# Kernel optimization log

Measured on AMD Instinct MI355X. Metric: run time of the kernel, lower is better.

## Reference

```python
import jax, jax.numpy as jnp
import numpy as np

N_NODES = 100000
N_EDGES = 1200000
IN_FEATS = 64
OUT_FEATS = 32
K_HOPS = 4  # k = len([in_feats] + hidden_lst) with hidden_lst=[64,64,32]


def setup_inputs() -> dict:
    key = jax.random.key(0)
    k1, k2, k3, k4, k5 = jax.random.split(key, 5)
    features = jax.random.normal(k1, (N_NODES, IN_FEATS), dtype=jnp.float32)
    src = jax.random.randint(k2, (N_EDGES,), 0, N_NODES, dtype=jnp.int64)
    dst = jax.random.randint(k3, (N_EDGES,), 0, N_NODES, dtype=jnp.int64)
    # fc layer of SGConv: Linear(in_feats -> out_feats) with bias
    bound = 1.0 / np.sqrt(IN_FEATS)
    W = jax.random.uniform(k4, (OUT_FEATS, IN_FEATS), dtype=jnp.float32,
                           minval=-bound, maxval=bound)
    b = jax.random.uniform(k5, (OUT_FEATS,), dtype=jnp.float32,
                           minval=-bound, maxval=bound)
    return {"features": features, "src": src, "dst": dst, "W": W, "b": b}


def reference(features, src, dst, W, b):
    # DGL SGConv with norm='both': symmetric normalization each hop.
    # in-degree of each dst node, clamped to >= 1
    deg = jax.ops.segment_sum(jnp.ones((N_EDGES,), dtype=features.dtype),
                              dst, num_segments=N_NODES)
    norm = jnp.clip(deg, 1.0, None) ** -0.5  # [N]
    norm = norm[:, None]                      # [N, 1]
    h = features
    for _ in range(K_HOPS):
        h = h * norm                                            # D^{-1/2} x
        h = jax.ops.segment_sum(h[src], dst, num_segments=N_NODES)  # A x (SpMM)
        h = h * norm                                            # D^{-1/2}
    # final linear layer
    return h @ W.T + b
```

## Files before the change

### kernel.cpp

```cpp
#include <hip/hip_runtime.h>
#include <hip/hip_fp16.h>
#include <cstdint>

#define NNODES 100000
#define NEDGES 1200000
#define INF 64
#define OUTF 32
#define SCAN_B 256
#define NBUCK ((NNODES + SCAN_B - 1) / SCAN_B)
#define PCAP 4608
#define PADCAP 5632
#define BIN_EPT 16
#define BIN_THREADS (NEDGES / BIN_EPT)
#define BIN_BLOCKS ((BIN_THREADS + 255) / 256)
#define PROJ_NPB 16
#define PROJ_BLOCKS (NNODES / PROJ_NPB)
#define CUR_PAD 16
#define WST 66

__global__ __launch_bounds__(256) void k_initcur(int* __restrict__ gcur,
                                                 uint4* __restrict__ h0,
                                                 uint4* __restrict__ h1) {
    int i = blockIdx.x * 256 + threadIdx.x;
    if (i < NBUCK) gcur[i * CUR_PAD] = i * PCAP;
    if (i >= 256 && i < 260) h0[(size_t)NNODES * 4 + (i - 256)] = make_uint4(0, 0, 0, 0);
    if (i >= 260 && i < 264) h1[(size_t)NNODES * 4 + (i - 260)] = make_uint4(0, 0, 0, 0);
}

__global__ __launch_bounds__(256) void k_binproj(const int4* __restrict__ src4,
                                                 const int4* __restrict__ dst4,
                                                 int* __restrict__ gcur,
                                                 unsigned* __restrict__ packed,
                                                 const float4* __restrict__ feat4,
                                                 const float4* __restrict__ W4,
                                                 __half2* __restrict__ h0_p) {
    __shared__ __align__(16) char smem[12672];
    int tid = threadIdx.x;
    if (blockIdx.x < BIN_BLOCKS) {
        int* cnt = (int*)smem;
        int* base = cnt + NBUCK;
        for (int i = tid; i < NBUCK; i += 256) cnt[i] = 0;
        __syncthreads();
        int gid = blockIdx.x * 256 + tid;
        bool act = gid < BIN_THREADS;
        int4 s4[4], d4[4];
        if (act) {
#pragma unroll
            for (int k = 0; k < 4; ++k) {
                s4[k] = src4[(size_t)gid * 4 + k];
                d4[k] = dst4[(size_t)gid * 4 + k];
                atomicAdd(&cnt[d4[k].x >> 8], 1);
                atomicAdd(&cnt[d4[k].y >> 8], 1);
                atomicAdd(&cnt[d4[k].z >> 8], 1);
                atomicAdd(&cnt[d4[k].w >> 8], 1);
            }
        }
        __syncthreads();
        for (int i = tid; i < NBUCK; i += 256) {
            int c = cnt[i];
            base[i] = c ? atomicAdd(&gcur[i * CUR_PAD], c) : 0;
            cnt[i] = 0;
        }
        __syncthreads();
        if (act) {
#pragma unroll
            for (int k = 0; k < 4; ++k) {
                int ss[4] = {s4[k].x, s4[k].y, s4[k].z, s4[k].w};
                int dd[4] = {d4[k].x, d4[k].y, d4[k].z, d4[k].w};
#pragma unroll
                for (int j = 0; j < 4; ++j) {
                    int b = dd[j] >> 8;
                    int rel = atomicAdd(&cnt[b], 1);
                    packed[base[b] + rel] =
                        ((unsigned)(dd[j] & 255) << 17) | (unsigned)ss[j];
                }
            }
        }
    } else {
        float (*Ws)[WST] = (float (*)[WST])smem;
        float (*Fs)[WST] = (float (*)[WST])(smem + 32 * WST * 4);
        int node0 = (blockIdx.x - BIN_BLOCKS) * PROJ_NPB;
        for (int i = tid; i < 512; i += 256) {
            float4 w = W4[i];
            int f = i * 4, of = f >> 6, k = f & 63;
            Ws[of][k] = w.x; Ws[of][k + 1] = w.y;
            Ws[of][k + 2] = w.z; Ws[of][k + 3] = w.w;
        }
        {
            int n = node0 + (tid >> 4), q = tid & 15;
            float4 v = feat4[(size_t)n * 16 + q];
            int c = q * 4;
            Fs[tid >> 4][c] = v.x; Fs[tid >> 4][c + 1] = v.y;
            Fs[tid >> 4][c + 2] = v.z; Fs[tid >> 4][c + 3] = v.w;
        }
        __syncthreads();
        int ln = tid >> 4, n = node0 + ln;
        int of0 = (tid & 15) * 2;
        const float2* fp = (const float2*)&Fs[ln][0];
        const float2* w0 = (const float2*)&Ws[of0][0];
        const float2* w1 = (const float2*)&Ws[of0 + 1][0];
        float a0 = 0.0f, a1 = 0.0f;
#pragma unroll
        for (int k2 = 0; k2 < 32; ++k2) {
            float2 f = fp[k2], x = w0[k2], y = w1[k2];
            a0 += f.x * x.x + f.y * x.y;
            a1 += f.x * y.x + f.y * y.y;
        }
        h0_p[(size_t)n * 16 + (tid & 15)] = __floats2half2_rn(a0, a1);
    }
}

__global__ __launch_bounds__(256) void k_place(const unsigned* __restrict__ packed,
                                               const int* __restrict__ gcur,
                                               int* __restrict__ col,
                                               unsigned* __restrict__ rowsd,
                                               float* __restrict__ norm,
                                               uint4* __restrict__ h0) {
    __shared__ unsigned sin_[PCAP];
    __shared__ int stage[PADCAP];
    __shared__ int deg[SCAN_B];
    __shared__ int rs[SCAN_B];
    __shared__ int cur[SCAN_B];
    __shared__ int tot;
    int b = blockIdx.x, tid = threadIdx.x;
    int node0 = b * SCAN_B;
    int nn = (NNODES - node0 < SCAN_B) ? (NNODES - node0) : SCAN_B;
    int ebase = b * PCAP;
    int pbase = b * PADCAP;
    int nedge = gcur[b * CUR_PAD] - ebase;
    deg[tid] = 0;
    __syncthreads();
    for (int i = tid; i < nedge; i += 256) {
        unsigned pk = packed[ebase + i];
        sin_[i] = pk;
        atomicAdd(&deg[pk >> 17], 1);
    }
    __syncthreads();
    int d = deg[tid];
    int dpad = (d + 7) & ~7;
    rs[tid] = dpad;
    __syncthreads();
    for (int st = 1; st < SCAN_B; st <<= 1) {
        int add = (tid >= st) ? rs[tid - st] : 0;
        __syncthreads();
        rs[tid] += add;
        __syncthreads();
    }
    int myoff = rs[tid] - dpad;
    if (tid == SCAN_B - 1) tot = rs[tid];
    float mynorm = rsqrtf(d < 1 ? 1.0f : (float)d);
    if (tid < nn) {
        norm[node0 + tid] = mynorm;
        rowsd[node0 + tid] =
            ((unsigned)((pbase + myoff) >> 3) << 9) | (unsigned)(dpad >> 3);
    }
    cur[tid] = myoff;
    __syncthreads();
    for (int i = tid; i < tot; i += 256) stage[i] = NNODES;
    __syncthreads();
    for (int i = tid; i < nedge; i += 256) {
        unsigned pk = sin_[i];
        int rel = atomicAdd(&cur[pk >> 17], 1);
        stage[rel] = (int)(pk & 0x1FFFFu);
    }
    __syncthreads();
    for (int i = tid; i < tot; i += 256) col[pbase + i] = stage[i];
    if (tid < nn) {
        uint4* hp = h0 + (size_t)(node0 + tid) * 4;
#pragma unroll
        for (int k = 0; k < 4; ++k) {
            uint4 r = hp[k];
            float2 f0 = __half22float2(*(const __half2*)&r.x);
            float2 f1 = __half22float2(*(const __half2*)&r.y);
            float2 f2 = __half22float2(*(const __half2*)&r.z);
            float2 f3 = __half22float2(*(const __half2*)&r.w);
            *(__half2*)&r.x = __floats2half2_rn(mynorm * f0.x, mynorm * f0.y);
            *(__half2*)&r.y = __floats2half2_rn(mynorm * f1.x, mynorm * f1.y);
            *(__half2*)&r.z = __floats2half2_rn(mynorm * f2.x, mynorm * f2.y);
            *(__half2*)&r.w = __floats2half2_rn(mynorm * f3.x, mynorm * f3.y);
            hp[k] = r;
        }
    }
}

template <bool LAST>
__global__ __launch_bounds__(256) void k_gather(const uint4* __restrict__ uin,
                                                void* __restrict__ uout,
                                                const unsigned* __restrict__ rowsd,
                                                const int4* __restrict__ colv,
                                                const float* __restrict__ norm,
                                                const float4* __restrict__ bias4) {
    int t = blockIdx.x * 256 + threadIdx.x;
    int node = t >> 2;
    if (node >= NNODES) return;
    int lane = t & 3;
    unsigned rd = rowsd[node];
    int c4 = (int)(rd >> 9) * 2;
    int n8 = (int)(rd & 511u);
    const uint4* up = uin + lane;
    float4 accA = make_float4(0.f, 0.f, 0.f, 0.f);
    float4 accB = make_float4(0.f, 0.f, 0.f, 0.f);
    auto add = [&](uint4 r) {
        float2 f0 = __half22float2(*(const __half2*)&r.x);
        float2 f1 = __half22float2(*(const __half2*)&r.y);
        float2 f2 = __half22float2(*(const __half2*)&r.z);
        float2 f3 = __half22float2(*(const __half2*)&r.w);
        accA.x += f0.x; accA.y += f0.y; accA.z += f1.x; accA.w += f1.y;
        accB.x += f2.x; accB.y += f2.y; accB.z += f3.x; accB.w += f3.y;
    };
    for (int j = 0; j < n8; ++j) {
        int4 c0 = colv[c4 + j * 2];
        int4 c1 = colv[c4 + j * 2 + 1];
        uint4 r0 = up[(size_t)c0.x * 4];
        uint4 r1 = up[(size_t)c0.y * 4];
        uint4 r2 = up[(size_t)c0.z * 4];
        uint4 r3 = up[(size_t)c0.w * 4];
        uint4 r4 = up[(size_t)c1.x * 4];
        uint4 r5 = up[(size_t)c1.y * 4];
        uint4 r6 = up[(size_t)c1.z * 4];
        uint4 r7 = up[(size_t)c1.w * 4];
        add(r0); add(r1); add(r2); add(r3);
        add(r4); add(r5); add(r6); add(r7);
    }
    float nn = norm[node];
    float w = LAST ? nn : nn * nn;
    accA.x *= w; accA.y *= w; accA.z *= w; accA.w *= w;
    accB.x *= w; accB.y *= w; accB.z *= w; accB.w *= w;
    if (LAST) {
        float4 b0 = bias4[lane * 2], b1 = bias4[lane * 2 + 1];
        accA.x += b0.x; accA.y += b0.y; accA.z += b0.z; accA.w += b0.w;
        accB.x += b1.x; accB.y += b1.y; accB.z += b1.z; accB.w += b1.w;
        float4* o = (float4*)uout;
        o[(size_t)node * 8 + lane * 2]     = accA;
        o[(size_t)node * 8 + lane * 2 + 1] = accB;
    } else {
        uint4 r;
        *(__half2*)&r.x = __floats2half2_rn(accA.x, accA.y);
        *(__half2*)&r.y = __floats2half2_rn(accA.z, accA.w);
        *(__half2*)&r.z = __floats2half2_rn(accB.x, accB.y);
        *(__half2*)&r.w = __floats2half2_rn(accB.z, accB.w);
        ((uint4*)uout)[(size_t)node * 4 + lane] = r;
    }
}

extern "C" void kernel_launch(void* const* d_in, const int* in_sizes, int n_in,
                              void* d_out, int out_size, void* d_ws, size_t ws_size,
                              hipStream_t stream) {
    const float* feat = (const float*)d_in[0];
    const int*   src  = (const int*)d_in[1];
    const int*   dst  = (const int*)d_in[2];
    const float* W    = (const float*)d_in[3];
    const float* b    = (const float*)d_in[4];
    float* out = (float*)d_out;

    char* ws = (char*)d_ws;
    size_t off = 0;
    auto alloc = [&](size_t bytes) {
        void* p = ws + off;
        off = (off + bytes + 255) & ~(size_t)255;
        return p;
    };
    float*    norm   = (float*)alloc((size_t)NNODES * 4);
    unsigned* rowsd  = (unsigned*)alloc((size_t)NNODES * 4);
    int*      gcur   = (int*)alloc((size_t)NBUCK * CUR_PAD * 4);
    unsigned* packed = (unsigned*)alloc((size_t)NBUCK * PCAP * 4);
    int*      col    = (int*)alloc((size_t)NBUCK * PADCAP * 4);
    void*     h0     = alloc((size_t)(NNODES + 1) * OUTF * 2);
    void*     h1     = alloc((size_t)(NNODES + 1) * OUTF * 2);

    k_initcur<<<2, 256, 0, stream>>>(gcur, (uint4*)h0, (uint4*)h1);
    k_binproj<<<BIN_BLOCKS + PROJ_BLOCKS, 256, 0, stream>>>(
        (const int4*)src, (const int4*)dst, gcur, packed,
        (const float4*)feat, (const float4*)W, (__half2*)h0);
    k_place<<<NBUCK, 256, 0, stream>>>(packed, gcur, col, rowsd, norm,
                                       (uint4*)h0);

    const int ggrid = (NNODES * 4 + 255) / 256;
    k_gather<false><<<ggrid, 256, 0, stream>>>(
        (const uint4*)h0, h1, rowsd, (const int4*)col, norm, nullptr);
    k_gather<false><<<ggrid, 256, 0, stream>>>(
        (const uint4*)h1, h0, rowsd, (const int4*)col, norm, nullptr);
    k_gather<false><<<ggrid, 256, 0, stream>>>(
        (const uint4*)h0, h1, rowsd, (const int4*)col, norm, nullptr);
    k_gather<true><<<ggrid, 256, 0, stream>>>(
        (const uint4*)h1, out, rowsd, (const int4*)col, norm, (const float4*)b);
}
```

Before: 119.6 us.

## Restage binning through shared memory and fuse projection with CSR placement

Binning now stages packed edges in shared memory, grouped per bucket, and writes them to global memory in contiguous runs instead of scattered stores. The feature projection moves from the binning kernel into the placement kernel, so it runs alongside CSR construction. The first gather applies the source norm per edge through a norm lookup, with a zero sentinel for padding, so the placement kernel no longer rescales h0. This aims to cut scattered writes and one read-modify-write pass over h0, at the cost of extra norm loads in the first hop and more shared memory in the binning kernel.

```diff
diff --git a/kernel.cpp b/kernel.cpp
--- a/kernel.cpp
+++ b/kernel.cpp
@@ -20,66 +20,131 @@
 
 __global__ __launch_bounds__(256) void k_initcur(int* __restrict__ gcur,
                                                  uint4* __restrict__ h0,
-                                                 uint4* __restrict__ h1) {
+                                                 uint4* __restrict__ h1,
+                                                 float* __restrict__ norm) {
     int i = blockIdx.x * 256 + threadIdx.x;
     if (i < NBUCK) gcur[i * CUR_PAD] = i * PCAP;
     if (i >= 256 && i < 260) h0[(size_t)NNODES * 4 + (i - 256)] = make_uint4(0, 0, 0, 0);
     if (i >= 260 && i < 264) h1[(size_t)NNODES * 4 + (i - 260)] = make_uint4(0, 0, 0, 0);
-}
-
-__global__ __launch_bounds__(256) void k_binproj(const int4* __restrict__ src4,
-                                                 const int4* __restrict__ dst4,
-                                                 int* __restrict__ gcur,
-                                                 unsigned* __restrict__ packed,
-                                                 const float4* __restrict__ feat4,
-                                                 const float4* __restrict__ W4,
-                                                 __half2* __restrict__ h0_p) {
-    __shared__ __align__(16) char smem[12672];
+    if (i == 264) norm[NNODES] = 0.0f;
+}
+
+__global__ __launch_bounds__(256) void k_bin(const int4* __restrict__ src4,
+                                             const int4* __restrict__ dst4,
+                                             int* __restrict__ gcur,
+                                             unsigned* __restrict__ packed) {
+    __shared__ int cnt[NBUCK];
+    __shared__ int base[NBUCK];
+    __shared__ int loff[NBUCK];
+    __shared__ int ltot;
+    __shared__ unsigned sval[4096];
+    __shared__ int saddr[4096];
     int tid = threadIdx.x;
-    if (blockIdx.x < BIN_BLOCKS) {
-        int* cnt = (int*)smem;
-        int* base = cnt + NBUCK;
-        for (int i = tid; i < NBUCK; i += 256) cnt[i] = 0;
-        __syncthreads();
-        int gid = blockIdx.x * 256 + tid;
-        bool act = gid < BIN_THREADS;
-        int4 s4[4], d4[4];
-        if (act) {
-#pragma unroll
-            for (int k = 0; k < 4; ++k) {
-                s4[k] = src4[(size_t)gid * 4 + k];
-                d4[k] = dst4[(size_t)gid * 4 + k];
-                atomicAdd(&cnt[d4[k].x >> 8], 1);
-                atomicAdd(&cnt[d4[k].y >> 8], 1);
-                atomicAdd(&cnt[d4[k].z >> 8], 1);
-                atomicAdd(&cnt[d4[k].w >> 8], 1);
+    for (int i = tid; i < NBUCK; i += 256) cnt[i] = 0;
+    if (tid == 0) ltot = 0;
+    __syncthreads();
+    int gid = blockIdx.x * 256 + tid;
+    bool act = gid < BIN_THREADS;
+    int4 s4[4], d4[4];
+    if (act) {
+#pragma unroll
+        for (int k = 0; k < 4; ++k) {
+            s4[k] = src4[(size_t)gid * 4 + k];
+            d4[k] = dst4[(size_t)gid * 4 + k];
+            atomicAdd(&cnt[d4[k].x >> 8], 1);
+            atomicAdd(&cnt[d4[k].y >> 8], 1);
+            atomicAdd(&cnt[d4[k].z >> 8], 1);
+            atomicAdd(&cnt[d4[k].w >> 8], 1);
+        }
+    }
+    __syncthreads();
+    for (int i = tid; i < NBUCK; i += 256) {
+        int c = cnt[i];
+        if (c) {
+            base[i] = atomicAdd(&gcur[i * CUR_PAD], c);
+            loff[i] = atomicAdd(&ltot, c);
+        }
+        cnt[i] = 0;
+    }
+    __syncthreads();
+    if (act) {
+#pragma unroll
+        for (int k = 0; k < 4; ++k) {
+            int ss[4] = {s4[k].x, s4[k].y, s4[k].z, s4[k].w};
+            int dd[4] = {d4[k].x, d4[k].y, d4[k].z, d4[k].w};
+#pragma unroll
+            for (int j = 0; j < 4; ++j) {
+                int b = dd[j] >> 8;
+                int rel = atomicAdd(&cnt[b], 1);
+                int p = loff[b] + rel;
+                sval[p] = ((unsigned)(dd[j] & 255) << 17) | (unsigned)ss[j];
+                saddr[p] = base[b] + rel;
             }
         }
-        __syncthreads();
-        for (int i = tid; i < NBUCK; i += 256) {
-            int c = cnt[i];
-            base[i] = c ? atomicAdd(&gcur[i * CUR_PAD], c) : 0;
-            cnt[i] = 0;
-        }
-        __syncthreads();
-        if (act) {
-#pragma unroll
-            for (int k = 0; k < 4; ++k) {
-                int ss[4] = {s4[k].x, s4[k].y, s4[k].z, s4[k].w};
-                int dd[4] = {d4[k].x, d4[k].y, d4[k].z, d4[k].w};
-#pragma unroll
-                for (int j = 0; j < 4; ++j) {
-                    int b = dd[j] >> 8;
-                    int rel = atomicAdd(&cnt[b], 1);
-                    packed[base[b] + rel] =
-                        ((unsigned)(dd[j] & 255) << 17) | (unsigned)ss[j];
-                }
-            }
-        }
+    }
+    __syncthreads();
+    int tot = ltot;
+    for (int i = tid; i < tot; i += 256) packed[saddr[i]] = sval[i];
+}
+
+__global__ __launch_bounds__(256) void k_placeproj(const unsigned* __restrict__ packed,
+                                                   const int* __restrict__ gcur,
+                                                   int* __restrict__ col,
+                                                   unsigned* __restrict__ rowsd,
+                                                   float* __restrict__ norm,
+                                                   const float4* __restrict__ feat4,
+                                                   const float4* __restrict__ W4,
+                                                   __half2* __restrict__ h0_p) {
+    __shared__ __align__(16) char smem[25664];
+    int tid = threadIdx.x;
+    if (blockIdx.x < NBUCK) {
+        int* stage = (int*)smem;
+        int* deg   = (int*)(smem + 22528);
+        int* rs    = (int*)(smem + 23552);
+        int* cur   = (int*)(smem + 24576);
+        int b = blockIdx.x;
+        int node0 = b * SCAN_B;
+        int nn = (NNODES - node0 < SCAN_B) ? (NNODES - node0) : SCAN_B;
+        int ebase = b * PCAP;
+        int pbase = b * PADCAP;
+        int nedge = gcur[b * CUR_PAD] - ebase;
+        deg[tid] = 0;
+        __syncthreads();
+        for (int i = tid; i < nedge; i += 256)
+            atomicAdd(&deg[packed[ebase + i] >> 17], 1);
+        __syncthreads();
+        int d = deg[tid];
+        int dpad = (d + 7) & ~7;
+        rs[tid] = dpad;
+        __syncthreads();
+        for (int st = 1; st < SCAN_B; st <<= 1) {
+            int add = (tid >= st) ? rs[tid - st] : 0;
+            __syncthreads();
+            rs[tid] += add;
+            __syncthreads();
+        }
+        int myoff = rs[tid] - dpad;
+        if (tid < nn) {
+            norm[node0 + tid] = rsqrtf(d < 1 ? 1.0f : (float)d);
+            rowsd[node0 + tid] =
+                ((unsigned)((pbase + myoff) >> 3) << 9) | (unsigned)(dpad >> 3);
+        }
+        cur[tid] = myoff;
+        __syncthreads();
+        int totp = rs[SCAN_B - 1];
+        for (int i = tid; i < totp; i += 256) stage[i] = NNODES;
+        __syncthreads();
+        for (int i = tid; i < nedge; i += 256) {
+            unsigned pk = packed[ebase + i];
+            int rel = atomicAdd(&cur[pk >> 17], 1);
+            stage[rel] = (int)(pk & 0x1FFFFu);
+        }
+        __syncthreads();
+        for (int i = tid; i < totp; i += 256) col[pbase + i] = stage[i];
     } else {
         float (*Ws)[WST] = (float (*)[WST])smem;
         float (*Fs)[WST] = (float (*)[WST])(smem + 32 * WST * 4);
-        int node0 = (blockIdx.x - BIN_BLOCKS) * PROJ_NPB;
+        int node0 = (blockIdx.x - NBUCK) * PROJ_NPB;
         for (int i = tid; i < 512; i += 256) {
             float4 w = W4[i];
             int f = i * 4, of = f >> 6, k = f & 63;
@@ -110,80 +175,7 @@
     }
 }
 
-__global__ __launch_bounds__(256) void k_place(const unsigned* __restrict__ packed,
-                                               const int* __restrict__ gcur,
-                                               int* __restrict__ col,
-                                               unsigned* __restrict__ rowsd,
-                                               float* __restrict__ norm,
-                                               uint4* __restrict__ h0) {
-    __shared__ unsigned sin_[PCAP];
-    __shared__ int stage[PADCAP];
-    __shared__ int deg[SCAN_B];
-    __shared__ int rs[SCAN_B];
-    __shared__ int cur[SCAN_B];
-    __shared__ int tot;
-    int b = blockIdx.x, tid = threadIdx.x;
-    int node0 = b * SCAN_B;
-    int nn = (NNODES - node0 < SCAN_B) ? (NNODES - node0) : SCAN_B;
-    int ebase = b * PCAP;
-    int pbase = b * PADCAP;
-    int nedge = gcur[b * CUR_PAD] - ebase;
-    deg[tid] = 0;
-    __syncthreads();
-    for (int i = tid; i < nedge; i += 256) {
-        unsigned pk = packed[ebase + i];
-        sin_[i] = pk;
-        atomicAdd(&deg[pk >> 17], 1);
-    }
-    __syncthreads();
-    int d = deg[tid];
-    int dpad = (d + 7) & ~7;
-    rs[tid] = dpad;
-    __syncthreads();
-    for (int st = 1; st < SCAN_B; st <<= 1) {
-        int add = (tid >= st) ? rs[tid - st] : 0;
-        __syncthreads();
-        rs[tid] += add;
-        __syncthreads();
-    }
-    int myoff = rs[tid] - dpad;
-    if (tid == SCAN_B - 1) tot = rs[tid];
-    float mynorm = rsqrtf(d < 1 ? 1.0f : (float)d);
-    if (tid < nn) {
-        norm[node0 + tid] = mynorm;
-        rowsd[node0 + tid] =
-            ((unsigned)((pbase + myoff) >> 3) << 9) | (unsigned)(dpad >> 3);
-    }
-    cur[tid] = myoff;
-    __syncthreads();
-    for (int i = tid; i < tot; i += 256) stage[i] = NNODES;
-    __syncthreads();
-    for (int i = tid; i < nedge; i += 256) {
-        unsigned pk = sin_[i];
-        int rel = atomicAdd(&cur[pk >> 17], 1);
-        stage[rel] = (int)(pk & 0x1FFFFu);
-    }
-    __syncthreads();
-    for (int i = tid; i < tot; i += 256) col[pbase + i] = stage[i];
-    if (tid < nn) {
-        uint4* hp = h0 + (size_t)(node0 + tid) * 4;
-#pragma unroll
-        for (int k = 0; k < 4; ++k) {
-            uint4 r = hp[k];
-            float2 f0 = __half22float2(*(const __half2*)&r.x);
-            float2 f1 = __half22float2(*(const __half2*)&r.y);
-            float2 f2 = __half22float2(*(const __half2*)&r.z);
-            float2 f3 = __half22float2(*(const __half2*)&r.w);
-            *(__half2*)&r.x = __floats2half2_rn(mynorm * f0.x, mynorm * f0.y);
-            *(__half2*)&r.y = __floats2half2_rn(mynorm * f1.x, mynorm * f1.y);
-            *(__half2*)&r.z = __floats2half2_rn(mynorm * f2.x, mynorm * f2.y);
-            *(__half2*)&r.w = __floats2half2_rn(mynorm * f3.x, mynorm * f3.y);
-            hp[k] = r;
-        }
-    }
-}
-
-template <bool LAST>
+template <bool FIRST, bool LAST>
 __global__ __launch_bounds__(256) void k_gather(const uint4* __restrict__ uin,
                                                 void* __restrict__ uout,
                                                 const unsigned* __restrict__ rowsd,
@@ -200,13 +192,13 @@
     const uint4* up = uin + lane;
     float4 accA = make_float4(0.f, 0.f, 0.f, 0.f);
     float4 accB = make_float4(0.f, 0.f, 0.f, 0.f);
-    auto add = [&](uint4 r) {
+    auto addw = [&](uint4 r, float w) {
         float2 f0 = __half22float2(*(const __half2*)&r.x);
         float2 f1 = __half22float2(*(const __half2*)&r.y);
         float2 f2 = __half22float2(*(const __half2*)&r.z);
         float2 f3 = __half22float2(*(const __half2*)&r.w);
-        accA.x += f0.x; accA.y += f0.y; accA.z += f1.x; accA.w += f1.y;
-        accB.x += f2.x; accB.y += f2.y; accB.z += f3.x; accB.w += f3.y;
+        accA.x += w * f0.x; accA.y += w * f0.y; accA.z += w * f1.x; accA.w += w * f1.y;
+        accB.x += w * f2.x; accB.y += w * f2.y; accB.z += w * f3.x; accB.w += w * f3.y;
     };
     for (int j = 0; j < n8; ++j) {
         int4 c0 = colv[c4 + j * 2];
@@ -219,8 +211,15 @@
         uint4 r5 = up[(size_t)c1.y * 4];
         uint4 r6 = up[(size_t)c1.z * 4];
         uint4 r7 = up[(size_t)c1.w * 4];
-        add(r0); add(r1); add(r2); add(r3);
-        add(r4); add(r5); add(r6); add(r7);
+        if (FIRST) {
+            addw(r0, norm[c0.x]); addw(r1, norm[c0.y]);
+            addw(r2, norm[c0.z]); addw(r3, norm[c0.w]);
+            addw(r4, norm[c1.x]); addw(r5, norm[c1.y]);
+            addw(r6, norm[c1.z]); addw(r7, norm[c1.w]);
+        } else {
+            addw(r0, 1.f); addw(r1, 1.f); addw(r2, 1.f); addw(r3, 1.f);
+            addw(r4, 1.f); addw(r5, 1.f); addw(r6, 1.f); addw(r7, 1.f);
+        }
     }
     float nn = norm[node];
     float w = LAST ? nn : nn * nn;
@@ -260,7 +259,7 @@
         off = (off + bytes + 255) & ~(size_t)255;
         return p;
     };
-    float*    norm   = (float*)alloc((size_t)NNODES * 4);
+    float*    norm   = (float*)alloc((size_t)(NNODES + 1) * 4);
     unsigned* rowsd  = (unsigned*)alloc((size_t)NNODES * 4);
     int*      gcur   = (int*)alloc((size_t)NBUCK * CUR_PAD * 4);
     unsigned* packed = (unsigned*)alloc((size_t)NBUCK * PCAP * 4);
@@ -268,20 +267,20 @@
     void*     h0     = alloc((size_t)(NNODES + 1) * OUTF * 2);
     void*     h1     = alloc((size_t)(NNODES + 1) * OUTF * 2);
 
-    k_initcur<<<2, 256, 0, stream>>>(gcur, (uint4*)h0, (uint4*)h1);
-    k_binproj<<<BIN_BLOCKS + PROJ_BLOCKS, 256, 0, stream>>>(
-        (const int4*)src, (const int4*)dst, gcur, packed,
+    k_initcur<<<2, 256, 0, stream>>>(gcur, (uint4*)h0, (uint4*)h1, norm);
+    k_bin<<<BIN_BLOCKS, 256, 0, stream>>>((const int4*)src, (const int4*)dst,
+                                          gcur, packed);
+    k_placeproj<<<NBUCK + PROJ_BLOCKS, 256, 0, stream>>>(
+        packed, gcur, col, rowsd, norm,
         (const float4*)feat, (const float4*)W, (__half2*)h0);
-    k_place<<<NBUCK, 256, 0, stream>>>(packed, gcur, col, rowsd, norm,
-                                       (uint4*)h0);
 
     const int ggrid = (NNODES * 4 + 255) / 256;
-    k_gather<false><<<ggrid, 256, 0, stream>>>(
+    k_gather<true,  false><<<ggrid, 256, 0, stream>>>(
         (const uint4*)h0, h1, rowsd, (const int4*)col, norm, nullptr);
-    k_gather<false><<<ggrid, 256, 0, stream>>>(
+    k_gather<false, false><<<ggrid, 256, 0, stream>>>(
         (const uint4*)h1, h0, rowsd, (const int4*)col, norm, nullptr);
-    k_gather<false><<<ggrid, 256, 0, stream>>>(
+    k_gather<false, false><<<ggrid, 256, 0, stream>>>(
         (const uint4*)h0, h1, rowsd, (const int4*)col, norm, nullptr);
-    k_gather<true><<<ggrid, 256, 0, stream>>>(
+    k_gather<false, true><<<ggrid, 256, 0, stream>>>(
         (const uint4*)h1, out, rowsd, (const int4*)col, norm, (const float4*)b);
 }
```

New measurement: 123.6 us. 1.03x slower.

## Split half-precision feature rows into two planes for cache-friendlier gathers

Applied to the files above, without the earlier changes.

Stores the 32-wide fp16 feature vectors as two separate 16-feature planes (32 bytes per node each) instead of one interleaved 64-byte row. Each gather block now handles one plane for 128 nodes, using two lanes per node, and adjacent blocks alternate planes. The intent is to halve the working set each gather touches, so random neighbour reads hit L2/MALL more often. The cost is that column indices and row metadata are read twice, once per plane, and each read is a smaller 32-byte segment.

```diff
diff --git a/kernel.cpp b/kernel.cpp
--- a/kernel.cpp
+++ b/kernel.cpp
@@ -17,14 +17,18 @@
 #define PROJ_BLOCKS (NNODES / PROJ_NPB)
 #define CUR_PAD 16
 #define WST 66
+#define PSTR4 ((size_t)(NNODES + 1) * 2)
+#define PSTRH ((size_t)(NNODES + 1) * 8)
 
 __global__ __launch_bounds__(256) void k_initcur(int* __restrict__ gcur,
                                                  uint4* __restrict__ h0,
                                                  uint4* __restrict__ h1) {
     int i = blockIdx.x * 256 + threadIdx.x;
     if (i < NBUCK) gcur[i * CUR_PAD] = i * PCAP;
-    if (i >= 256 && i < 260) h0[(size_t)NNODES * 4 + (i - 256)] = make_uint4(0, 0, 0, 0);
-    if (i >= 260 && i < 264) h1[(size_t)NNODES * 4 + (i - 260)] = make_uint4(0, 0, 0, 0);
+    if (i >= 256 && i < 258) h0[(size_t)NNODES * 2 + (i - 256)] = make_uint4(0, 0, 0, 0);
+    if (i >= 258 && i < 260) h0[PSTR4 + (size_t)NNODES * 2 + (i - 258)] = make_uint4(0, 0, 0, 0);
+    if (i >= 260 && i < 262) h1[(size_t)NNODES * 2 + (i - 260)] = make_uint4(0, 0, 0, 0);
+    if (i >= 262 && i < 264) h1[PSTR4 + (size_t)NNODES * 2 + (i - 262)] = make_uint4(0, 0, 0, 0);
 }
 
 __global__ __launch_bounds__(256) void k_binproj(const int4* __restrict__ src4,
@@ -95,7 +99,8 @@
         }
         __syncthreads();
         int ln = tid >> 4, n = node0 + ln;
-        int of0 = (tid & 15) * 2;
+        int q = tid & 15;
+        int of0 = q * 2;
         const float2* fp = (const float2*)&Fs[ln][0];
         const float2* w0 = (const float2*)&Ws[of0][0];
         const float2* w1 = (const float2*)&Ws[of0 + 1][0];
@@ -106,7 +111,8 @@
             a0 += f.x * x.x + f.y * x.y;
             a1 += f.x * y.x + f.y * y.y;
         }
-        h0_p[(size_t)n * 16 + (tid & 15)] = __floats2half2_rn(a0, a1);
+        h0_p[(size_t)(q >> 3) * PSTRH + (size_t)n * 8 + (q & 7)] =
+            __floats2half2_rn(a0, a1);
     }
 }
 
@@ -166,19 +172,24 @@
     __syncthreads();
     for (int i = tid; i < tot; i += 256) col[pbase + i] = stage[i];
     if (tid < nn) {
-        uint4* hp = h0 + (size_t)(node0 + tid) * 4;
-#pragma unroll
-        for (int k = 0; k < 4; ++k) {
-            uint4 r = hp[k];
-            float2 f0 = __half22float2(*(const __half2*)&r.x);
-            float2 f1 = __half22float2(*(const __half2*)&r.y);
-            float2 f2 = __half22float2(*(const __half2*)&r.z);
-            float2 f3 = __half22float2(*(const __half2*)&r.w);
-            *(__half2*)&r.x = __floats2half2_rn(mynorm * f0.x, mynorm * f0.y);
-            *(__half2*)&r.y = __floats2half2_rn(mynorm * f1.x, mynorm * f1.y);
-            *(__half2*)&r.z = __floats2half2_rn(mynorm * f2.x, mynorm * f2.y);
-            *(__half2*)&r.w = __floats2half2_rn(mynorm * f3.x, mynorm * f3.y);
-            hp[k] = r;
+        uint4* hp0 = h0 + (size_t)(node0 + tid) * 2;
+        uint4* hp1 = h0 + PSTR4 + (size_t)(node0 + tid) * 2;
+        uint4* hp[2] = {hp0, hp1};
+#pragma unroll
+        for (int pl = 0; pl < 2; ++pl) {
+#pragma unroll
+            for (int k = 0; k < 2; ++k) {
+                uint4 r = hp[pl][k];
+                float2 f0 = __half22float2(*(const __half2*)&r.x);
+                float2 f1 = __half22float2(*(const __half2*)&r.y);
+                float2 f2 = __half22float2(*(const __half2*)&r.z);
+                float2 f3 = __half22float2(*(const __half2*)&r.w);
+                *(__half2*)&r.x = __floats2half2_rn(mynorm * f0.x, mynorm * f0.y);
+                *(__half2*)&r.y = __floats2half2_rn(mynorm * f1.x, mynorm * f1.y);
+                *(__half2*)&r.z = __floats2half2_rn(mynorm * f2.x, mynorm * f2.y);
+                *(__half2*)&r.w = __floats2half2_rn(mynorm * f3.x, mynorm * f3.y);
+                hp[pl][k] = r;
+            }
         }
     }
 }
@@ -190,14 +201,15 @@
                                                 const int4* __restrict__ colv,
                                                 const float* __restrict__ norm,
                                                 const float4* __restrict__ bias4) {
-    int t = blockIdx.x * 256 + threadIdx.x;
-    int node = t >> 2;
+    int bid = blockIdx.x;
+    int h = bid & 1;
+    int node = (bid >> 1) * 128 + (threadIdx.x >> 1);
     if (node >= NNODES) return;
-    int lane = t & 3;
+    int lane = threadIdx.x & 1;
     unsigned rd = rowsd[node];
     int c4 = (int)(rd >> 9) * 2;
     int n8 = (int)(rd & 511u);
-    const uint4* up = uin + lane;
+    const uint4* up = uin + (size_t)h * PSTR4 + lane;
     float4 accA = make_float4(0.f, 0.f, 0.f, 0.f);
     float4 accB = make_float4(0.f, 0.f, 0.f, 0.f);
     auto add = [&](uint4 r) {
@@ -211,14 +223,14 @@
     for (int j = 0; j < n8; ++j) {
         int4 c0 = colv[c4 + j * 2];
         int4 c1 = colv[c4 + j * 2 + 1];
-        uint4 r0 = up[(size_t)c0.x * 4];
-        uint4 r1 = up[(size_t)c0.y * 4];
-        uint4 r2 = up[(size_t)c0.z * 4];
-        uint4 r3 = up[(size_t)c0.w * 4];
-        uint4 r4 = up[(size_t)c1.x * 4];
-        uint4 r5 = up[(size_t)c1.y * 4];
-        uint4 r6 = up[(size_t)c1.z * 4];
-        uint4 r7 = up[(size_t)c1.w * 4];
+        uint4 r0 = up[(size_t)c0.x * 2];
+        uint4 r1 = up[(size_t)c0.y * 2];
+        uint4 r2 = up[(size_t)c0.z * 2];
+        uint4 r3 = up[(size_t)c0.w * 2];
+        uint4 r4 = up[(size_t)c1.x * 2];
+        uint4 r5 = up[(size_t)c1.y * 2];
+        uint4 r6 = up[(size_t)c1.z * 2];
+        uint4 r7 = up[(size_t)c1.w * 2];
         add(r0); add(r1); add(r2); add(r3);
         add(r4); add(r5); add(r6); add(r7);
     }
@@ -227,19 +239,19 @@
     accA.x *= w; accA.y *= w; accA.z *= w; accA.w *= w;
     accB.x *= w; accB.y *= w; accB.z *= w; accB.w *= w;
     if (LAST) {
-        float4 b0 = bias4[lane * 2], b1 = bias4[lane * 2 + 1];
+        float4 b0 = bias4[h * 4 + lane * 2], b1 = bias4[h * 4 + lane * 2 + 1];
         accA.x += b0.x; accA.y += b0.y; accA.z += b0.z; accA.w += b0.w;
         accB.x += b1.x; accB.y += b1.y; accB.z += b1.z; accB.w += b1.w;
         float4* o = (float4*)uout;
-        o[(size_t)node * 8 + lane * 2]     = accA;
-        o[(size_t)node * 8 + lane * 2 + 1] = accB;
+        o[(size_t)node * 8 + h * 4 + lane * 2]     = accA;
+        o[(size_t)node * 8 + h * 4 + lane * 2 + 1] = accB;
     } else {
         uint4 r;
         *(__half2*)&r.x = __floats2half2_rn(accA.x, accA.y);
         *(__half2*)&r.y = __floats2half2_rn(accA.z, accA.w);
         *(__half2*)&r.z = __floats2half2_rn(accB.x, accB.y);
         *(__half2*)&r.w = __floats2half2_rn(accB.z, accB.w);
-        ((uint4*)uout)[(size_t)node * 4 + lane] = r;
+        ((uint4*)uout)[(size_t)h * PSTR4 + (size_t)node * 2 + lane] = r;
     }
 }
 
@@ -275,7 +287,7 @@
     k_place<<<NBUCK, 256, 0, stream>>>(packed, gcur, col, rowsd, norm,
                                        (uint4*)h0);
 
-    const int ggrid = (NNODES * 4 + 255) / 256;
+    const int ggrid = ((NNODES + 127) / 128) * 2;
     k_gather<false><<<ggrid, 256, 0, stream>>>(
         (const uint4*)h0, h1, rowsd, (const int4*)col, norm, nullptr);
     k_gather<false><<<ggrid, 256, 0, stream>>>(
```

Result: slower. 134.2 us (+12.2%).
